# Optimization experiments

Hardware: AMD Instinct MI355X
Metric: run time of the kernel (lower is better)

The kernel has to match this reference:

```python
import jax, jax.numpy as jnp
import numpy as np

# Forest of B complete binary trees: L leaves, NPT = 2L-1 nodes per tree.
B, L, H = 128, 512, 128
NPT = 2 * L - 1
N = B * NPT
VOCAB, OUT = 32000, 128


def _levels():
    """Static topo schedule: per internal level, (node, left_child, right_child) global ids."""
    tree_off = np.arange(B, dtype=np.int32)[:, None] * NPT  # [B,1]
    levels = []
    off, cnt = 0, L
    while cnt > 1:
        child_off = off
        off += cnt
        cnt //= 2
        node = off + np.arange(cnt, dtype=np.int32)
        left = child_off + 2 * np.arange(cnt, dtype=np.int32)
        right = left + 1
        levels.append(tuple(jnp.asarray((a[None, :] + tree_off).ravel())
                            for a in (node, left, right)))
    roots = jnp.asarray((tree_off[:, 0] + (NPT - 1)).astype(np.int32))
    leaves = jnp.asarray((np.arange(L, dtype=np.int32)[None, :] + tree_off).ravel())
    return levels, roots, leaves


def setup_inputs() -> dict:
    key = jax.random.key(0)
    ks = jax.random.split(key, 8)
    s = lambda k, shp, sc: jax.random.normal(k, shp, jnp.float32) * sc
    return {
        "label": jax.random.randint(ks[0], (N,), 0, VOCAB),
        "emb": s(ks[1], (VOCAB, H), 0.02),
        "W_iou": s(ks[2], (H, 3 * H), H ** -0.5),
        "U_iou": s(ks[3], (2 * H, 3 * H), (2 * H) ** -0.5),
        "b_iou": jnp.zeros((3 * H,), jnp.float32),
        "U_f_w": s(ks[4], (2 * H, 2 * H), (2 * H) ** -0.5),
        "U_f_b": jnp.zeros((2 * H,), jnp.float32),
        "W_out": s(ks[5], (H, OUT), H ** -0.5),
        "b_out": jnp.zeros((OUT,), jnp.float32),
    }


def _apply_node(iou, b_iou, c_in):
    # apply_node_func: gates + LSTM cell update
    i, o, u = jnp.split(iou + b_iou, 3, axis=-1)
    c = jax.nn.sigmoid(i) * jnp.tanh(u) + c_in
    h = jax.nn.sigmoid(o) * jnp.tanh(c)
    return h, c


def reference(label, emb, W_iou, U_iou, b_iou, U_f_w, U_f_b, W_out, b_out):
    levels, roots, leaves = _levels()
    iou0 = emb[label] @ W_iou                      # [N, 3H] W_iou(emb(label)) for every node
    h = jnp.zeros((N, H), iou0.dtype)
    c = jnp.zeros((N, H), iou0.dtype)
    # leaves: no incoming messages, c_in = 0
    hl, cl = _apply_node(iou0[leaves], b_iou, 0.0)
    h = h.at[leaves].set(hl)
    c = c.at[leaves].set(cl)
    # internal frontiers in topological order (fan-in = 2)
    for node, left, right in levels:
        h_cat = jnp.concatenate([h[left], h[right]], axis=-1)   # [n_d, 2H]
        f = jax.nn.sigmoid(h_cat @ U_f_w + U_f_b)               # forget gates per child
        fl, fr = jnp.split(f, 2, axis=-1)
        c_red = fl * c[left] + fr * c[right]                    # child-sum of gated cells
        iou = h_cat @ U_iou                                     # reduce_func overwrites iou
        hn, cn = _apply_node(iou, b_iou, c_red)
        h = h.at[node].set(hn)
        c = c.at[node].set(cn)
    final = h[roots] @ W_out + b_out                            # root hidden per tree
    return jax.nn.log_softmax(final, axis=-1)
```

## Files before the change

### kernel.cpp

```cpp
#include <hip/hip_runtime.h>
#include <math.h>

#define B_    128
#define L_    512
#define H_    128
#define NPT_  1023
#define N_    (B_ * NPT_)
#define NLEAF (B_ * L_)
#define OUT_  128
#define VOCAB 32000
#define TBASE 960
#define BROW  264

typedef unsigned short ushort_t;
typedef __attribute__((ext_vector_type(8))) __bf16 bf16x8;
typedef __attribute__((ext_vector_type(4))) float f32x4;

__device__ __forceinline__ float sigmoidf_(float x) {
    return 1.0f / (1.0f + __expf(-x));
}
__device__ __forceinline__ float tanhf_(float x) {
    return 1.0f - 2.0f / (__expf(2.0f * x) + 1.0f);
}
__device__ __forceinline__ ushort_t f2bf(float f) {
    unsigned u = __float_as_uint(f);
    return (ushort_t)((u + 0x7fffu + ((u >> 16) & 1u)) >> 16);
}
__device__ __forceinline__ float bf2f(ushort_t s) {
    return __uint_as_float(((unsigned)s) << 16);
}

__global__ __launch_bounds__(256)
void prep_fused(const float* __restrict__ W_iou,
                const float* __restrict__ U_iou,
                const float* __restrict__ U_f_w,
                const float* __restrict__ emb,
                ushort_t* __restrict__ W_iouT,
                ushort_t* __restrict__ U_catT,
                ushort_t* __restrict__ embb) {
    int idx = blockIdx.x * 256 + threadIdx.x;
    if (idx < VOCAB * H_ / 8) {
        int e0 = idx * 8;
        f32x4 f0 = *(const f32x4*)(emb + e0);
        f32x4 f1 = *(const f32x4*)(emb + e0 + 4);
        union { bf16x8 v; ushort_t e[8]; } p;
        p.e[0] = f2bf(f0[0]); p.e[1] = f2bf(f0[1]);
        p.e[2] = f2bf(f0[2]); p.e[3] = f2bf(f0[3]);
        p.e[4] = f2bf(f1[0]); p.e[5] = f2bf(f1[1]);
        p.e[6] = f2bf(f1[2]); p.e[7] = f2bf(f1[3]);
        *(bf16x8*)(embb + e0) = p.v;
    }
    if (idx < 640 * 256) {
        int n = idx >> 8, k = idx & 255;
        float v = (n < 384) ? U_iou[k * 384 + n] : U_f_w[k * 256 + (n - 384)];
        U_catT[idx] = f2bf(v);
    }
    if (idx < 384 * 128) {
        int n = idx >> 7, k = idx & 127;
        W_iouT[idx] = f2bf(W_iou[k * 384 + n]);
    }
}

__global__ __launch_bounds__(256, 4)
void leaf_v3(const int* __restrict__ label,
             const ushort_t* __restrict__ embb,
             const ushort_t* __restrict__ WT,
             const float* __restrict__ b_iou,
             ushort_t* __restrict__ h,
             float* __restrict__ c) {
    const int tid  = threadIdx.x;
    const int lane = tid & 63;
    const int wave = tid >> 6;
    const int li   = lane & 15;
    const int q    = lane >> 4;
    const int q8   = q << 3;
    const int gg   = blockIdx.y * 4 + wave;
    const int j    = gg * 16 + li;

    bf16x8 Bf[3][4];
    #pragma unroll
    for (int t = 0; t < 3; ++t) {
        const ushort_t* bp = WT + (size_t)(16 * (gg + 8 * t) + li) * 128 + q8;
        #pragma unroll
        for (int kt = 0; kt < 4; ++kt) Bf[t][kt] = *(const bf16x8*)(bp + kt * 32);
    }

    int lab[8];
    #pragma unroll
    for (int t = 0; t < 8; ++t) {
        int ia = (blockIdx.x + t * 512) * 16 + li;
        int ba = ia >> 9, pa = ia & 511;
        lab[t] = label[ba * NPT_ + pa];
    }

    const float bi = b_iou[j], bo = b_iou[128 + j], bu = b_iou[256 + j];

    #pragma unroll 1
    for (int t8 = 0; t8 < 8; ++t8) {
        const int tile = blockIdx.x + t8 * 512;
        const int i0 = tile * 16;
        const ushort_t* pA = embb + (size_t)lab[t8] * H_;
        bf16x8 a[4];
        #pragma unroll
        for (int kt = 0; kt < 4; ++kt) a[kt] = *(const bf16x8*)(pA + kt * 32 + q8);

        f32x4 acc[3];
        #pragma unroll
        for (int t = 0; t < 3; ++t) acc[t] = (f32x4){0.f, 0.f, 0.f, 0.f};
        #pragma unroll
        for (int kt = 0; kt < 4; ++kt)
            #pragma unroll
            for (int t = 0; t < 3; ++t)
                acc[t] = __builtin_amdgcn_mfma_f32_16x16x32_bf16(a[kt], Bf[t][kt], acc[t], 0, 0, 0);

        #pragma unroll
        for (int r = 0; r < 4; ++r) {
            int m  = i0 + q * 4 + r;
            int b  = m >> 9, pos = m & 511;
            size_t gn = (size_t)(b * NPT_ + pos) * H_ + j;
            float iv = sigmoidf_(acc[0][r] + bi);
            float ov = sigmoidf_(acc[1][r] + bo);
            float uv = tanhf_(acc[2][r] + bu);
            float cv = iv * uv;
            float hv = ov * tanhf_(cv);
            c[gn] = cv;
            h[gn] = f2bf(hv);
        }
    }
}

__global__ __launch_bounds__(256, 2)
void level_lds(const ushort_t* __restrict__ Ucat,
               const float* __restrict__ b_iou,
               const float* __restrict__ U_f_b,
               ushort_t* __restrict__ h,
               float* __restrict__ c,
               int node_base, int child_base, int lc, int ntiles) {
    __shared__ ushort_t Bs[5 * 16 * BROW];
    const int tid  = threadIdx.x;
    const int lane = tid & 63;
    const int wave = tid >> 6;
    const int li   = lane & 15;
    const int q    = lane >> 4;
    const int q8   = q << 3;
    const int mask = (1 << lc) - 1;
    const int gg   = blockIdx.y;
    const int j    = gg * 16 + li;

    #pragma unroll
    for (int it = 0; it < 5; ++it) {
        int chunk = tid + it * 256;
        int row = chunk >> 4, seg = chunk & 15;
        int t = row >> 4, lr = row & 15;
        const ushort_t* src = Ucat + (size_t)(16 * (gg + 8 * t) + lr) * 256 + seg * 16;
        ushort_t*       dst = Bs + (t * 16 + lr) * BROW + seg * 16;
        *(f32x4*)(dst)     = *(const f32x4*)(src);
        *(f32x4*)(dst + 8) = *(const f32x4*)(src + 8);
    }
    __syncthreads();

    const float bi  = b_iou[j], bo = b_iou[128 + j], bu = b_iou[256 + j];
    const float bfl = U_f_b[j], bfr = U_f_b[128 + j];
    const int wstride = gridDim.x * 4;

    #pragma unroll 1
    for (int tile = blockIdx.x * 4 + wave; tile < ntiles; tile += wstride) {
        const int i0 = tile * 16;

        float clv[4], crv[4];
        int   gnrow[4];
        #pragma unroll
        for (int r = 0; r < 4; ++r) {
            int m = i0 + q * 4 + r;
            int b = m >> lc, pos = m & mask;
            int gl = b * NPT_ + child_base + 2 * pos;
            gnrow[r] = b * NPT_ + node_base + pos;
            clv[r] = c[(size_t)gl * H_ + j];
            crv[r] = c[(size_t)(gl + 1) * H_ + j];
        }

        int ia = i0 + li, ba = ia >> lc, pa = ia & mask;
        int gl0 = ba * NPT_ + child_base + 2 * pa;
        const ushort_t* pl = h + (size_t)gl0 * H_;
        const ushort_t* pr = h + (size_t)(gl0 + 1) * H_;
        bf16x8 a[8];
        #pragma unroll
        for (int kt = 0; kt < 8; ++kt) {
            const ushort_t* p = (kt < 4) ? pl : pr;
            a[kt] = *(const bf16x8*)(p + (kt & 3) * 32 + q8);
        }

        f32x4 acc[5];
        #pragma unroll
        for (int t = 0; t < 5; ++t) acc[t] = (f32x4){0.f, 0.f, 0.f, 0.f};
        #pragma unroll
        for (int kt = 0; kt < 8; ++kt) {
            #pragma unroll
            for (int t = 0; t < 5; ++t) {
                bf16x8 bf = *(const bf16x8*)(Bs + (t * 16 + li) * BROW + kt * 32 + q8);
                acc[t] = __builtin_amdgcn_mfma_f32_16x16x32_bf16(a[kt], bf, acc[t], 0, 0, 0);
            }
        }

        #pragma unroll
        for (int r = 0; r < 4; ++r) {
            size_t gn = (size_t)gnrow[r] * H_ + j;
            float iv = sigmoidf_(acc[0][r] + bi);
            float ov = sigmoidf_(acc[1][r] + bo);
            float uv = tanhf_(acc[2][r] + bu);
            float fl = sigmoidf_(acc[3][r] + bfl);
            float fr = sigmoidf_(acc[4][r] + bfr);
            float cv = iv * uv + fl * clv[r] + fr * crv[r];
            float hv = ov * tanhf_(cv);
            c[gn] = cv;
            h[gn] = f2bf(hv);
        }
    }
}

#define TPAD 132
__global__ __launch_bounds__(512, 2)
void tail_kernel(const ushort_t* __restrict__ Ucat,
                 const float* __restrict__ b_iou,
                 const float* __restrict__ U_f_b,
                 const ushort_t* __restrict__ h,
                 const float* __restrict__ c,
                 const float* __restrict__ W_out,
                 const float* __restrict__ b_out,
                 float* __restrict__ out) {
    __shared__ ushort_t hl[63][TPAD];
    __shared__ float    cl[63][TPAD];
    __shared__ float    ev[H_];
    __shared__ float    red[128];
    __shared__ float    red4[4][128];

    const int tid  = threadIdx.x;
    const int lane = tid & 63;
    const int wave = tid >> 6;
    const int li   = lane & 15;
    const int q    = lane >> 4;
    const int q8   = q << 3;
    const int gg   = wave;
    const int j    = gg * 16 + li;
    const int b    = blockIdx.x;

    bf16x8 Bf[5][8];
    #pragma unroll
    for (int t = 0; t < 5; ++t) {
        const ushort_t* bp = Ucat + (size_t)(16 * (gg + 8 * t) + li) * 256 + q8;
        #pragma unroll
        for (int kt = 0; kt < 8; ++kt) Bf[t][kt] = *(const bf16x8*)(bp + kt * 32);
    }

    const float bi  = b_iou[j], bo = b_iou[128 + j], bu = b_iou[256 + j];
    const float bfl = U_f_b[j], bfr = U_f_b[128 + j];

    int base = TBASE, child = 896, cnt = 32;
    #pragma unroll 1
    for (int lvl = 0; lvl < 6; ++lvl) {
        const int tiles = (cnt + 15) >> 4;
        for (int tile = 0; tile < tiles; ++tile) {
            const int i0 = tile * 16;

            int pos = i0 + li; if (pos >= cnt) pos = cnt - 1;
            bf16x8 a[8];
            if (lvl == 0) {
                int gl0 = b * NPT_ + child + 2 * pos;
                const ushort_t* pl = h + (size_t)gl0 * H_;
                const ushort_t* pr = h + (size_t)(gl0 + 1) * H_;
                #pragma unroll
                for (int kt = 0; kt < 8; ++kt) {
                    const ushort_t* p = (kt < 4) ? pl : pr;
                    a[kt] = *(const bf16x8*)(p + (kt & 3) * 32 + q8);
                }
            } else {
                int tl = (child - TBASE) + 2 * pos;
                #pragma unroll
                for (int kt = 0; kt < 8; ++kt) {
                    const ushort_t* p = (kt < 4) ? hl[tl] : hl[tl + 1];
                    a[kt] = *(const bf16x8*)(p + (kt & 3) * 32 + q8);
                }
            }

            float clv[4], crv[4];
            #pragma unroll
            for (int r = 0; r < 4; ++r) {
                int m  = i0 + q * 4 + r;
                int pm = m < cnt ? m : cnt - 1;
                if (lvl == 0) {
                    int gl = b * NPT_ + child + 2 * pm;
                    clv[r] = c[(size_t)gl * H_ + j];
                    crv[r] = c[(size_t)(gl + 1) * H_ + j];
                } else {
                    int tl = (child - TBASE) + 2 * pm;
                    clv[r] = cl[tl][j];
                    crv[r] = cl[tl + 1][j];
                }
            }

            f32x4 acc[5];
            #pragma unroll
            for (int t = 0; t < 5; ++t) acc[t] = (f32x4){0.f, 0.f, 0.f, 0.f};
            #pragma unroll
            for (int kt = 0; kt < 8; ++kt)
                #pragma unroll
                for (int t = 0; t < 5; ++t)
                    acc[t] = __builtin_amdgcn_mfma_f32_16x16x32_bf16(a[kt], Bf[t][kt], acc[t], 0, 0, 0);

            #pragma unroll
            for (int r = 0; r < 4; ++r) {
                int m = i0 + q * 4 + r;
                if (m < cnt) {
                    int tl = (base - TBASE) + m;
                    float iv = sigmoidf_(acc[0][r] + bi);
                    float ov = sigmoidf_(acc[1][r] + bo);
                    float uv = tanhf_(acc[2][r] + bu);
                    float fl = sigmoidf_(acc[3][r] + bfl);
                    float fr = sigmoidf_(acc[4][r] + bfr);
                    float cv = iv * uv + fl * clv[r] + fr * crv[r];
                    float hv = ov * tanhf_(cv);
                    cl[tl][j] = cv;
                    hl[tl][j] = f2bf(hv);
                }
            }
        }
        __syncthreads();
        child = base; base += cnt; cnt >>= 1;
    }

    if (tid < 128) ev[tid] = bf2f(hl[62][tid]);
    __syncthreads();

    {
        const int o  = tid & 127;
        const int kc = tid >> 7;
        float pacc = (kc == 0) ? b_out[o] : 0.0f;
        #pragma unroll 8
        for (int k = kc * 32; k < kc * 32 + 32; ++k)
            pacc += ev[k] * W_out[k * OUT_ + o];
        red4[kc][o] = pacc;
    }
    __syncthreads();

    float acc = 0.0f;
    if (tid < 128) {
        acc = red4[0][tid] + red4[1][tid] + red4[2][tid] + red4[3][tid];
        red[tid] = acc;
    }
    __syncthreads();
    for (int s = 64; s > 0; s >>= 1) {
        if (tid < s) red[tid] = fmaxf(red[tid], red[tid + s]);
        __syncthreads();
    }
    float mx = red[0];
    __syncthreads();
    if (tid < 128) red[tid] = expf(acc - mx);
    __syncthreads();
    for (int s = 64; s > 0; s >>= 1) {
        if (tid < s) red[tid] += red[tid + s];
        __syncthreads();
    }
    float lse = logf(red[0]);
    if (tid < 128) out[b * OUT_ + tid] = acc - mx - lse;
}

extern "C" void kernel_launch(void* const* d_in, const int* in_sizes, int n_in,
                              void* d_out, int out_size, void* d_ws, size_t ws_size,
                              hipStream_t stream) {
    const int*   label = (const int*)d_in[0];
    const float* emb   = (const float*)d_in[1];
    const float* W_iou = (const float*)d_in[2];
    const float* U_iou = (const float*)d_in[3];
    const float* b_iou = (const float*)d_in[4];
    const float* U_f_w = (const float*)d_in[5];
    const float* U_f_b = (const float*)d_in[6];
    const float* W_out = (const float*)d_in[7];
    const float* b_out = (const float*)d_in[8];
    float* outp = (float*)d_out;

    float*    c    = (float*)d_ws;
    ushort_t* h    = (ushort_t*)(c + (size_t)N_ * H_);
    ushort_t* Ucat = h + (size_t)N_ * H_;
    ushort_t* WT   = Ucat + 640 * 256;
    ushort_t* embb = WT + 384 * 128;

    prep_fused<<<2000, 256, 0, stream>>>(W_iou, U_iou, U_f_w, emb, WT, Ucat, embb);

    leaf_v3<<<dim3(512, 2), 256, 0, stream>>>(label, embb, WT, b_iou, h, c);

    int child = 0, node = 512, cnt = 256, lc = 8;
    for (int lvl = 0; lvl < 3; ++lvl) {
        int ntiles  = (B_ * cnt) / 16;
        int stripes = ntiles / 16;
        level_lds<<<dim3(stripes, 8), 256, 0, stream>>>(
            Ucat, b_iou, U_f_b, h, c, node, child, lc, ntiles);
        child = node; node += cnt; cnt >>= 1; --lc;
    }

    tail_kernel<<<B_, 512, 0, stream>>>(Ucat, b_iou, U_f_b, h, c, W_out, b_out, outp);
}
```

Before: 198.9 us.

## Fuse three tree-level kernels into one cooperative kernel with grid syncs

```diff
diff --git a/kernel.cpp b/kernel.cpp
--- a/kernel.cpp
+++ b/kernel.cpp
@@ -1,5 +1,8 @@
 #include <hip/hip_runtime.h>
+#include <hip/hip_cooperative_groups.h>
 #include <math.h>
+
+namespace cg = cooperative_groups;
 
 #define B_    128
 #define L_    512
@@ -130,21 +133,22 @@
 }
 
 __global__ __launch_bounds__(256, 2)
-void level_lds(const ushort_t* __restrict__ Ucat,
-               const float* __restrict__ b_iou,
-               const float* __restrict__ U_f_b,
-               ushort_t* __restrict__ h,
-               float* __restrict__ c,
-               int node_base, int child_base, int lc, int ntiles) {
+void levels_fused(const ushort_t* __restrict__ Ucat,
+                  const float* __restrict__ b_iou,
+                  const float* __restrict__ U_f_b,
+                  ushort_t* __restrict__ h,
+                  float* __restrict__ c) {
     __shared__ ushort_t Bs[5 * 16 * BROW];
+    cg::grid_group grid = cg::this_grid();
+
     const int tid  = threadIdx.x;
     const int lane = tid & 63;
     const int wave = tid >> 6;
     const int li   = lane & 15;
     const int q    = lane >> 4;
     const int q8   = q << 3;
-    const int mask = (1 << lc) - 1;
-    const int gg   = blockIdx.y;
+    const int gg   = blockIdx.x >> 6;
+    const int sid  = blockIdx.x & 63;
     const int j    = gg * 16 + li;
 
     #pragma unroll
@@ -161,60 +165,72 @@
 
     const float bi  = b_iou[j], bo = b_iou[128 + j], bu = b_iou[256 + j];
     const float bfl = U_f_b[j], bfr = U_f_b[128 + j];
-    const int wstride = gridDim.x * 4;
-
+
+    int child = 0, node = 512, cnt = 256, lc = 8;
     #pragma unroll 1
-    for (int tile = blockIdx.x * 4 + wave; tile < ntiles; tile += wstride) {
-        const int i0 = tile * 16;
-
-        float clv[4], crv[4];
-        int   gnrow[4];
-        #pragma unroll
-        for (int r = 0; r < 4; ++r) {
-            int m = i0 + q * 4 + r;
-            int b = m >> lc, pos = m & mask;
-            int gl = b * NPT_ + child_base + 2 * pos;
-            gnrow[r] = b * NPT_ + node_base + pos;
-            clv[r] = c[(size_t)gl * H_ + j];
-            crv[r] = c[(size_t)(gl + 1) * H_ + j];
+    for (int lvl = 0; lvl < 3; ++lvl) {
+        const int mask   = (1 << lc) - 1;
+        const int ntiles = (B_ * cnt) >> 4;
+
+        #pragma unroll 1
+        for (int tile = sid * 4 + wave; tile < ntiles; tile += 256) {
+            const int i0 = tile * 16;
+
+            float clv[4], crv[4];
+            int   gnrow[4];
+            #pragma unroll
+            for (int r = 0; r < 4; ++r) {
+                int m = i0 + q * 4 + r;
+                int b = m >> lc, pos = m & mask;
+                int gl = b * NPT_ + child + 2 * pos;
+                gnrow[r] = b * NPT_ + node + pos;
+                clv[r] = c[(size_t)gl * H_ + j];
+                crv[r] = c[(size_t)(gl + 1) * H_ + j];
+            }
+
+            int ia = i0 + li, ba = ia >> lc, pa = ia & mask;
+            int gl0 = ba * NPT_ + child + 2 * pa;
+            const ushort_t* pl = h + (size_t)gl0 * H_;
+            const ushort_t* pr = h + (size_t)(gl0 + 1) * H_;
+            bf16x8 a[8];
+            #pragma unroll
+            for (int kt = 0; kt < 8; ++kt) {
+                const ushort_t* p = (kt < 4) ? pl : pr;
+                a[kt] = *(const bf16x8*)(p + (kt & 3) * 32 + q8);
+            }
+
+            f32x4 acc[5];
+            #pragma unroll
+            for (int t = 0; t < 5; ++t) acc[t] = (f32x4){0.f, 0.f, 0.f, 0.f};
+            #pragma unroll
+            for (int kt = 0; kt < 8; ++kt) {
+                #pragma unroll
+                for (int t = 0; t < 5; ++t) {
+                    bf16x8 bf = *(const bf16x8*)(Bs + (t * 16 + li) * BROW + kt * 32 + q8);
+                    acc[t] = __builtin_amdgcn_mfma_f32_16x16x32_bf16(a[kt], bf, acc[t], 0, 0, 0);
+                }
+            }
+
+            #pragma unroll
+            for (int r = 0; r < 4; ++r) {
+                size_t gn = (size_t)gnrow[r] * H_ + j;
+                float iv = sigmoidf_(acc[0][r] + bi);
+                float ov = sigmoidf_(acc[1][r] + bo);
+                float uv = tanhf_(acc[2][r] + bu);
+                float fl = sigmoidf_(acc[3][r] + bfl);
+                float fr = sigmoidf_(acc[4][r] + bfr);
+                float cv = iv * uv + fl * clv[r] + fr * crv[r];
+                float hv = ov * tanhf_(cv);
+                c[gn] = cv;
+                h[gn] = f2bf(hv);
+            }
         }
 
-        int ia = i0 + li, ba = ia >> lc, pa = ia & mask;
-        int gl0 = ba * NPT_ + child_base + 2 * pa;
-        const ushort_t* pl = h + (size_t)gl0 * H_;
-        const ushort_t* pr = h + (size_t)(gl0 + 1) * H_;
-        bf16x8 a[8];
-        #pragma unroll
-        for (int kt = 0; kt < 8; ++kt) {
-            const ushort_t* p = (kt < 4) ? pl : pr;
-            a[kt] = *(const bf16x8*)(p + (kt & 3) * 32 + q8);
+        if (lvl != 2) {
+            __threadfence();
+            grid.sync();
         }
-
-        f32x4 acc[5];
-        #pragma unroll
-        for (int t = 0; t < 5; ++t) acc[t] = (f32x4){0.f, 0.f, 0.f, 0.f};
-        #pragma unroll
-        for (int kt = 0; kt < 8; ++kt) {
-            #pragma unroll
-            for (int t = 0; t < 5; ++t) {
-                bf16x8 bf = *(const bf16x8*)(Bs + (t * 16 + li) * BROW + kt * 32 + q8);
-                acc[t] = __builtin_amdgcn_mfma_f32_16x16x32_bf16(a[kt], bf, acc[t], 0, 0, 0);
-            }
-        }
-
-        #pragma unroll
-        for (int r = 0; r < 4; ++r) {
-            size_t gn = (size_t)gnrow[r] * H_ + j;
-            float iv = sigmoidf_(acc[0][r] + bi);
-            float ov = sigmoidf_(acc[1][r] + bo);
-            float uv = tanhf_(acc[2][r] + bu);
-            float fl = sigmoidf_(acc[3][r] + bfl);
-            float fr = sigmoidf_(acc[4][r] + bfr);
-            float cv = iv * uv + fl * clv[r] + fr * crv[r];
-            float hv = ov * tanhf_(cv);
-            c[gn] = cv;
-            h[gn] = f2bf(hv);
-        }
+        child = node; node += cnt; cnt >>= 1; --lc;
     }
 }
 
@@ -388,13 +404,11 @@
 
     leaf_v3<<<dim3(512, 2), 256, 0, stream>>>(label, embb, WT, b_iou, h, c);
 
-    int child = 0, node = 512, cnt = 256, lc = 8;
-    for (int lvl = 0; lvl < 3; ++lvl) {
-        int ntiles  = (B_ * cnt) / 16;
-        int stripes = ntiles / 16;
-        level_lds<<<dim3(stripes, 8), 256, 0, stream>>>(
-            Ucat, b_iou, U_f_b, h, c, node, child, lc, ntiles);
-        child = node; node += cnt; cnt >>= 1; --lc;
+    {
+        void* kargs[] = { (void*)&Ucat, (void*)&b_iou, (void*)&U_f_b,
+                          (void*)&h, (void*)&c };
+        hipLaunchCooperativeKernel((const void*)levels_fused,
+                                   dim3(512), dim3(256), kargs, 0, stream);
     }
 
     tail_kernel<<<B_, 512, 0, stream>>>(Ucat, b_iou, U_f_b, h, c, W_out, b_out, outp);
```

Result: slower. 454.7 us (+128.7%).
